# Performance work log

Hardware: AMD Instinct MI355X
Metric: run time of the kernel (lower is better)

## Reference

```python
import jax, jax.numpy as jnp
import numpy as np

N_LAYERS = 12
N_HEADS = 12
D_MODEL = 768
VOCAB = 50257
T_WIN = 1024
B, T = 4, 1024
STD = 0.02


def setup_inputs() -> dict:
    key = jax.random.key(0)
    ks = jax.random.split(key, 8)
    inp = jax.random.randint(ks[0], (B, T), 0, VOCAB)
    target = jax.random.randint(ks[1], (B, T), 0, VOCAB)
    wte = jax.random.normal(ks[2], (VOCAB, D_MODEL), jnp.float32) * STD
    wpe = jax.random.normal(ks[3], (T_WIN, D_MODEL), jnp.float32) * STD
    attn_w = jax.random.normal(ks[4], (N_LAYERS, D_MODEL, 3 * D_MODEL), jnp.float32) * STD
    proj_w = jax.random.normal(ks[5], (N_LAYERS, D_MODEL, D_MODEL), jnp.float32) * STD
    fc_w = jax.random.normal(ks[6], (N_LAYERS, D_MODEL, 4 * D_MODEL), jnp.float32) * STD
    fc2_w = jax.random.normal(ks[7], (N_LAYERS, 4 * D_MODEL, D_MODEL), jnp.float32) * STD
    return {
        'inp': inp, 'target': target, 'wte': wte, 'wpe': wpe,
        'ln1_w': jnp.ones((N_LAYERS, D_MODEL), jnp.float32),
        'ln1_b': jnp.zeros((N_LAYERS, D_MODEL), jnp.float32),
        'attn_w': attn_w,
        'attn_b': jnp.zeros((N_LAYERS, 3 * D_MODEL), jnp.float32),
        'proj_w': proj_w,
        'proj_b': jnp.zeros((N_LAYERS, D_MODEL), jnp.float32),
        'ln2_w': jnp.ones((N_LAYERS, D_MODEL), jnp.float32),
        'ln2_b': jnp.zeros((N_LAYERS, D_MODEL), jnp.float32),
        'fc_w': fc_w,
        'fc_b': jnp.zeros((N_LAYERS, 4 * D_MODEL), jnp.float32),
        'fc2_w': fc2_w,
        'fc2_b': jnp.zeros((N_LAYERS, D_MODEL), jnp.float32),
        'lnf_w': jnp.ones((D_MODEL,), jnp.float32),
        'lnf_b': jnp.zeros((D_MODEL,), jnp.float32),
    }


def _layernorm(x, w, b, eps=1e-5):
    mu = jnp.mean(x, axis=-1, keepdims=True)
    var = jnp.var(x, axis=-1, keepdims=True)
    return (x - mu) * jax.lax.rsqrt(var + eps) * w + b


def _attention(x, w_qkv, b_qkv, w_proj, b_proj):
    b, t, c = x.shape
    hd = c // N_HEADS
    qkv = x @ w_qkv + b_qkv                      # [B,T,3C]
    q, k, v = jnp.split(qkv, 3, axis=-1)
    # [B,H,T,hd]
    q = q.reshape(b, t, N_HEADS, hd).transpose(0, 2, 1, 3)
    k = k.reshape(b, t, N_HEADS, hd).transpose(0, 2, 1, 3)
    v = v.reshape(b, t, N_HEADS, hd).transpose(0, 2, 1, 3)
    scores = jnp.einsum('bhqd,bhkd->bhqk', q, k) / jnp.sqrt(jnp.float32(hd))
    causal = jnp.tril(jnp.ones((t, t), bool))
    scores = jnp.where(causal[None, None], scores, -jnp.inf)
    w = jax.nn.softmax(scores, axis=-1)          # dropout p=0 (eval)
    ctx = jnp.einsum('bhqk,bhkd->bhqd', w, v)
    ctx = ctx.transpose(0, 2, 1, 3).reshape(b, t, c)
    return ctx @ w_proj + b_proj


def reference(inp, target, wte, wpe, ln1_w, ln1_b, attn_w, attn_b, proj_w, proj_b,
              ln2_w, ln2_b, fc_w, fc_b, fc2_w, fc2_b, lnf_w, lnf_b):
    b, t = inp.shape
    x = wte[inp] + wpe[:t][None]                 # [B,T,C]
    for i in range(N_LAYERS):
        x = x + _attention(_layernorm(x, ln1_w[i], ln1_b[i]),
                           attn_w[i], attn_b[i], proj_w[i], proj_b[i])
        h = _layernorm(x, ln2_w[i], ln2_b[i])
        h = jax.nn.gelu(h @ fc_w[i] + fc_b[i], approximate=True)
        x = x + (h @ fc2_w[i] + fc2_b[i])
    x = _layernorm(x, lnf_w, lnf_b)
    logits = x @ wte.T                            # tied lm_head, no bias
    logp = jax.nn.log_softmax(logits, axis=-1)
    nll = -jnp.take_along_axis(logp, target[..., None], axis=-1)[..., 0]
    loss = jnp.mean(nll)
    return logits, loss
```

## Files before the change

kernel.cpp:

```cpp
#include <hip/hip_runtime.h>
#include <hip/hip_bf16.h>
#include <cmath>

#define NLAYERS 12
#define NHEADS  12
#define DM      768
#define VOCAB   50257
#define TSEQ    1024
#define BT      4096
#define NCHUNK  786

typedef __attribute__((ext_vector_type(4))) float f32x4;
typedef __attribute__((ext_vector_type(8))) short bf16x8;
typedef __attribute__((ext_vector_type(4))) short s16x4;

typedef __hip_bfloat16 bf16;

#define MFMA16(a, b, c) __builtin_amdgcn_mfma_f32_16x16x32_bf16(a, b, c, 0, 0, 0)

__device__ __forceinline__ void gload16(const void* g, void* l) {
    __builtin_amdgcn_global_load_lds(
        (const __attribute__((address_space(1))) void*)g,
        (__attribute__((address_space(3))) void*)l, 16, 0, 0);
}

__device__ __forceinline__ void wg_barrier() {
    asm volatile("" ::: "memory");
    __builtin_amdgcn_s_barrier();
    asm volatile("" ::: "memory");
}

__device__ __forceinline__ float gelu_tanh(float v) {
    float u = 0.7978845608028654f * (v + 0.044715f * v * v * v);
    return 0.5f * v * (1.0f + tanhf(u));
}

__device__ __forceinline__ short f2bf(float f) {
    bf16 h = (bf16)f;
    return *reinterpret_cast<short*>(&h);
}

struct ushort4s { short a, b, c, d; };

__global__ void transpose_bf16_kernel(const float* __restrict__ in, bf16* __restrict__ out,
                                      int K, int N) {
    __shared__ float tile[32][33];
    size_t lofs = (size_t)blockIdx.z * K * N;
    int k0 = blockIdx.y * 32, n0 = blockIdx.x * 32;
    int tx = threadIdx.x, ty = threadIdx.y;
#pragma unroll
    for (int i = 0; i < 32; i += 8)
        tile[ty + i][tx] = in[lofs + (size_t)(k0 + ty + i) * N + n0 + tx];
    __syncthreads();
#pragma unroll
    for (int i = 0; i < 32; i += 8)
        out[lofs + (size_t)(n0 + ty + i) * K + k0 + tx] = (bf16)tile[tx][ty + i];
}

__global__ void tobf16_kernel(const float* __restrict__ in, bf16* __restrict__ out, size_t n) {
    size_t i = (size_t)blockIdx.x * 256 + threadIdx.x;
    if (i < n) out[i] = (bf16)in[i];
}

__global__ void embed_kernel(const int* __restrict__ inp, const float* __restrict__ wte,
                             const float* __restrict__ wpe, float* __restrict__ x) {
    int idx = blockIdx.x * 256 + threadIdx.x;
    int m = idx / (DM / 4), c4 = idx % (DM / 4);
    int tok = inp[m];
    int t = m & (TSEQ - 1);
    float4 a = reinterpret_cast<const float4*>(wte)[(size_t)tok * (DM / 4) + c4];
    float4 b = reinterpret_cast<const float4*>(wpe)[(size_t)t * (DM / 4) + c4];
    float4 o = {a.x + b.x, a.y + b.y, a.z + b.z, a.w + b.w};
    reinterpret_cast<float4*>(x)[idx] = o;
}

__global__ __launch_bounds__(256) void ln_kernel(const float* __restrict__ x,
                                                 const float* __restrict__ w,
                                                 const float* __restrict__ b,
                                                 bf16* __restrict__ y) {
    int tid = threadIdx.x, wv = tid >> 6, lane = tid & 63;
    int row = blockIdx.x * 4 + wv;
    const float4* xr = reinterpret_cast<const float4*>(x + (size_t)row * DM);
    float4 v[3];
    float s = 0.f, q = 0.f;
#pragma unroll
    for (int j = 0; j < 3; ++j) {
        v[j] = xr[lane + 64 * j];
        s += v[j].x + v[j].y + v[j].z + v[j].w;
        q += v[j].x * v[j].x + v[j].y * v[j].y + v[j].z * v[j].z + v[j].w * v[j].w;
    }
#pragma unroll
    for (int o = 1; o < 64; o <<= 1) { s += __shfl_xor(s, o); q += __shfl_xor(q, o); }
    float mu  = s * (1.0f / DM);
    float var = q * (1.0f / DM) - mu * mu;
    float inv = rsqrtf(var + 1e-5f);
#pragma unroll
    for (int j = 0; j < 3; ++j) {
        int c4 = lane + 64 * j;
        float4 wv4 = reinterpret_cast<const float4*>(w)[c4];
        float4 bv4 = reinterpret_cast<const float4*>(b)[c4];
        ushort4s o;
        o.a = f2bf((v[j].x - mu) * inv * wv4.x + bv4.x);
        o.b = f2bf((v[j].y - mu) * inv * wv4.y + bv4.y);
        o.c = f2bf((v[j].z - mu) * inv * wv4.z + bv4.z);
        o.d = f2bf((v[j].w - mu) * inv * wv4.w + bv4.w);
        *reinterpret_cast<ushort4s*>(y + (size_t)row * DM + c4 * 4) = o;
    }
}

#define GF_GELU    1
#define GF_OBF16   2
#define GF_CLAMP   4
#define GF_PARTIAL 8

template<int FLAGS, int TAG>
__global__ __launch_bounds__(256) void gemm_k(
    const bf16* __restrict__ A, const bf16* __restrict__ Bt,
    const float* __restrict__ bias, const float* __restrict__ resid,
    void* __restrict__ C, float2* __restrict__ partials,
    int M, int N, int K) {
    __shared__ short ldsA[2][128 * 32];
    __shared__ short ldsB[2][128 * 32];
    int tid = threadIdx.x;
    int lane = tid & 63, w = tid >> 6;
    int wm = w >> 1, wn = w & 1;
    int r = lane & 15, kq = lane >> 4;
    int bm = blockIdx.x * 128, bn = blockIdx.y * 128;

    f32x4 acc[4][4] = {};

    auto stage = [&](int buf, int k0) {
#pragma unroll
        for (int i = 0; i < 2; ++i) {
            int chunk = i * 256 + tid;
            int row = chunk >> 2;
            int gs = (chunk & 3) ^ ((row >> 1) & 3);
            const bf16* ga = A + (size_t)(bm + row) * K + k0 + gs * 8;
            gload16(ga, &ldsA[buf][(i * 256 + w * 64) * 8]);
            int brow = bn + row;
            if (FLAGS & GF_CLAMP) brow = min(brow, N - 1);
            const bf16* gb = Bt + (size_t)brow * K + k0 + gs * 8;
            gload16(gb, &ldsB[buf][(i * 256 + w * 64) * 8]);
        }
    };
    auto compute = [&](int buf) {
        bf16x8 af[4], bfr[4];
#pragma unroll
        for (int m = 0; m < 4; ++m) {
            int row = wm * 64 + m * 16 + r;
            af[m] = *reinterpret_cast<bf16x8*>(&ldsA[buf][row * 32 + (kq ^ ((row >> 1) & 3)) * 8]);
        }
#pragma unroll
        for (int n = 0; n < 4; ++n) {
            int row = wn * 64 + n * 16 + r;
            bfr[n] = *reinterpret_cast<bf16x8*>(&ldsB[buf][row * 32 + (kq ^ ((row >> 1) & 3)) * 8]);
        }
#pragma unroll
        for (int m = 0; m < 4; ++m)
#pragma unroll
            for (int n = 0; n < 4; ++n)
                acc[m][n] = MFMA16(af[m], bfr[n], acc[m][n]);
    };

    stage(0, 0);
    __syncthreads();
    int buf = 0;
    for (int k0 = 32; k0 < K; k0 += 32) {
        stage(buf ^ 1, k0);
        compute(buf);
        __syncthreads();
        buf ^= 1;
    }
    compute(buf);

    int row0 = bm + wm * 64, col0 = bn + wn * 64;
#pragma unroll
    for (int m = 0; m < 4; ++m) {
#pragma unroll
        for (int n = 0; n < 4; ++n) {
            int col = col0 + n * 16 + r;
            if (col < N) {
#pragma unroll
                for (int rr = 0; rr < 4; ++rr) {
                    int row = row0 + m * 16 + kq * 4 + rr;
                    float v = acc[m][n][rr];
                    if (bias) v += bias[col];
                    if (FLAGS & GF_GELU) v = gelu_tanh(v);
                    if (resid) v += resid[(size_t)row * N + col];
                    if (FLAGS & GF_OBF16) ((bf16*)C)[(size_t)row * N + col] = (bf16)v;
                    else                  ((float*)C)[(size_t)row * N + col] = v;
                }
            }
        }
    }
}

template<int FLAGS, int TAG>
__global__ __launch_bounds__(512, 1) void gemm256_8p(
    const bf16* __restrict__ A, const bf16* __restrict__ Bt,
    const float* __restrict__ bias, const float* __restrict__ resid,
    void* __restrict__ C, float2* __restrict__ partials,
    int M, int N, int K) {
    __shared__ short lds[2][2][256 * 64];
    int tid = threadIdx.x;
    int lane = tid & 63, w = tid >> 6;
    int wm = w >> 2, wn = w & 3;
    int r = lane & 15, kq = lane >> 4;
    int bm = blockIdx.x * 256, bn = blockIdx.y * 256;

    f32x4 acc[8][4] = {};

    auto stage_half = [&](int buf, int kt, int half) {
        int mat = half >> 1;
        int hrow = (half & 1) * 128;
        const bf16* src = mat ? Bt : A;
        int base = mat ? bn : bm;
#pragma unroll
        for (int i = 0; i < 2; ++i) {
            int chunk = i * 512 + tid;
            int lrow = hrow + (chunk >> 3);
            int gsrc = (chunk & 7) ^ (lrow & 7);
            int grow = base + lrow;
            if (mat && (FLAGS & GF_CLAMP)) grow = min(grow, N - 1);
            gload16(src + (size_t)grow * K + kt * 64 + gsrc * 8,
                    &lds[buf][mat][hrow * 64 + chunk * 8]);
        }
    };

    auto do_phase = [&](int buf, int p) {
        int mh = p >> 1, nh = p & 1;
        bf16x8 bfr[2][2], af[4][2];
#pragma unroll
        for (int n2 = 0; n2 < 2; ++n2) {
            int row = wn * 64 + (nh * 2 + n2) * 16 + r;
#pragma unroll
            for (int kk = 0; kk < 2; ++kk)
                bfr[n2][kk] = *reinterpret_cast<bf16x8*>(
                    &lds[buf][1][row * 64 + ((kk * 4 + kq) ^ (row & 7)) * 8]);
        }
#pragma unroll
        for (int m2 = 0; m2 < 4; ++m2) {
            int row = wm * 128 + (mh * 4 + m2) * 16 + r;
#pragma unroll
            for (int kk = 0; kk < 2; ++kk)
                af[m2][kk] = *reinterpret_cast<bf16x8*>(
                    &lds[buf][0][row * 64 + ((kk * 4 + kq) ^ (row & 7)) * 8]);
        }
        __builtin_amdgcn_s_setprio(1);
#pragma unroll
        for (int m2 = 0; m2 < 4; ++m2)
#pragma unroll
            for (int n2 = 0; n2 < 2; ++n2)
#pragma unroll
                for (int kk = 0; kk < 2; ++kk)
                    acc[mh * 4 + m2][nh * 2 + n2] =
                        MFMA16(af[m2][kk], bfr[n2][kk], acc[mh * 4 + m2][nh * 2 + n2]);
        __builtin_amdgcn_s_setprio(0);
    };

    const int NT = K / 64;
    stage_half(0, 0, 0); stage_half(0, 0, 1); stage_half(0, 0, 2); stage_half(0, 0, 3);
    for (int t = 0; t < NT; ++t) {
        int buf = t & 1;
        bool more = (t + 1 < NT);
        if (more) { stage_half(buf ^ 1, t + 1, 0); stage_half(buf ^ 1, t + 1, 1); }
        if (more) asm volatile("s_waitcnt vmcnt(4)" ::: "memory");
        else      asm volatile("s_waitcnt vmcnt(0)" ::: "memory");
        wg_barrier();
        do_phase(buf, 0);
        wg_barrier();
        if (more) { stage_half(buf ^ 1, t + 1, 2); stage_half(buf ^ 1, t + 1, 3); }
        do_phase(buf, 1);
        wg_barrier();
        do_phase(buf, 2);
        wg_barrier();
        do_phase(buf, 3);
        wg_barrier();
    }

    int row0 = bm + wm * 128, col0 = bn + wn * 64;
#pragma unroll
    for (int m = 0; m < 8; ++m) {
#pragma unroll
        for (int n = 0; n < 4; ++n) {
            int col = col0 + n * 16 + r;
            if (col < N) {
#pragma unroll
                for (int rr = 0; rr < 4; ++rr) {
                    int row = row0 + m * 16 + kq * 4 + rr;
                    float v = acc[m][n][rr];
                    if (bias) v += bias[col];
                    if (FLAGS & GF_GELU) v = gelu_tanh(v);
                    if (resid) v += resid[(size_t)row * N + col];
                    if (FLAGS & GF_OBF16) ((bf16*)C)[(size_t)row * N + col] = (bf16)v;
                    else                  ((float*)C)[(size_t)row * N + col] = v;
                }
            }
        }
    }

    if (FLAGS & GF_PARTIAL) {
        int chunk = (bn >> 6) + wn;
        if (chunk < NCHUNK) {
#pragma unroll
            for (int m = 0; m < 8; ++m) {
#pragma unroll
                for (int rr = 0; rr < 4; ++rr) {
                    float vals[4], mx = -INFINITY;
#pragma unroll
                    for (int n = 0; n < 4; ++n) {
                        int col = col0 + n * 16 + r;
                        float v = (col < N) ? acc[m][n][rr] : -INFINITY;
                        vals[n] = v;
                        mx = fmaxf(mx, v);
                    }
#pragma unroll
                    for (int o = 1; o < 16; o <<= 1) mx = fmaxf(mx, __shfl_xor(mx, o));
                    float sum = 0.f;
#pragma unroll
                    for (int n = 0; n < 4; ++n)
                        if (vals[n] > -INFINITY) sum += __expf(vals[n] - mx);
#pragma unroll
                    for (int o = 1; o < 16; o <<= 1) sum += __shfl_xor(sum, o);
                    if (r == 0) {
                        int row = row0 + m * 16 + kq * 4 + rr;
                        partials[(size_t)row * NCHUNK + chunk] = make_float2(mx, sum);
                    }
                }
            }
        }
    }
}

__global__ __launch_bounds__(256) void flash_attn_kernel(const bf16* __restrict__ qkv,
                                                         bf16* __restrict__ ctx) {
    __shared__ short Ks[128 * 64];
    __shared__ short Vt[64 * 128];
    __shared__ short Ps[4][16][132];

    int tid = threadIdx.x, lane = tid & 63, w = tid >> 6;
    int r = lane & 15, kq = lane >> 4;
    int q0 = blockIdx.x * 64;
    int bh = blockIdx.y;
    int b = bh / NHEADS, h = bh % NHEADS;
    const int RS = 3 * DM;

    const bf16* qbase = qkv + (size_t)(b * TSEQ + q0 + w * 16 + r) * RS + h * 64;
    bf16x8 qf[2];
    qf[0] = *reinterpret_cast<const bf16x8*>(qbase + kq * 8);
    qf[1] = *reinterpret_cast<const bf16x8*>(qbase + 32 + kq * 8);

    f32x4 of[4] = {};
    float mrow[4] = {-INFINITY, -INFINITY, -INFINITY, -INFINITY};
    float lrow[4] = {};

    int kvq = tid >> 3;
    int d0 = (tid & 7) * 8;
    const bf16* kbase0 = qkv + (size_t)(b * TSEQ) * RS + DM + h * 64;
    const bf16* vbase0 = qkv + (size_t)(b * TSEQ) * RS + 2 * DM + h * 64;
    bf16x8 kr0, kr1, kr2, kr3, vr0, vr1, vr2, vr3;

    auto loadKV = [&](int t) {
        const bf16* kb = kbase0 + (size_t)(t * 128 + kvq * 4) * RS + d0;
        const bf16* vb = vbase0 + (size_t)(t * 128 + kvq * 4) * RS + d0;
        kr0 = *reinterpret_cast<const bf16x8*>(kb);
        kr1 = *reinterpret_cast<const bf16x8*>(kb + RS);
        kr2 = *reinterpret_cast<const bf16x8*>(kb + 2 * RS);
        kr3 = *reinterpret_cast<const bf16x8*>(kb + 3 * RS);
        vr0 = *reinterpret_cast<const bf16x8*>(vb);
        vr1 = *reinterpret_cast<const bf16x8*>(vb + RS);
        vr2 = *reinterpret_cast<const bf16x8*>(vb + 2 * RS);
        vr3 = *reinterpret_cast<const bf16x8*>(vb + 3 * RS);
    };
    auto writeKV = [&]() {
        bf16x8 krs[4] = {kr0, kr1, kr2, kr3};
#pragma unroll
        for (int j = 0; j < 4; ++j) {
            int kv = kvq * 4 + j;
            int pg = (tid & 7) ^ (kv & 7);
            *reinterpret_cast<bf16x8*>(&Ks[kv * 64 + pg * 8]) = krs[j];
        }
        int lg = kvq >> 1, half = kvq & 1;
#pragma unroll
        for (int jj = 0; jj < 8; ++jj) {
            int d = d0 + jj;
            int phys = lg ^ (d & 7);
            s16x4 pk = {vr0[jj], vr1[jj], vr2[jj], vr3[jj]};
            *reinterpret_cast<s16x4*>(&Vt[d * 128 + phys * 8 + half * 4]) = pk;
        }
    };

    int ntiles = (blockIdx.x >> 1) + 1;
    loadKV(0);
    for (int t = 0; t < ntiles; ++t) {
        __syncthreads();
        writeKV();
        __syncthreads();
        if (t + 1 < ntiles) loadKV(t + 1);

        int kv0 = t * 128;
        f32x4 sf[8];
#pragma unroll
        for (int n = 0; n < 8; ++n) sf[n] = (f32x4){0.f, 0.f, 0.f, 0.f};
        __builtin_amdgcn_s_setprio(1);
#pragma unroll
        for (int n = 0; n < 8; ++n) {
            int row = n * 16 + r;
#pragma unroll
            for (int kt = 0; kt < 2; ++kt) {
                int gran = (kt * 4 + kq) ^ (row & 7);
                bf16x8 kf = *reinterpret_cast<bf16x8*>(&Ks[row * 64 + gran * 8]);
                sf[n] = MFMA16(qf[kt], kf, sf[n]);
            }
        }
        __builtin_amdgcn_s_setprio(0);

        bool diag = (kv0 + 128 > q0);
        float alpha[4];
#pragma unroll
        for (int rr = 0; rr < 4; ++rr) {
            int qrow = q0 + w * 16 + kq * 4 + rr;
            float vals[8];
            float mx = mrow[rr];
#pragma unroll
            for (int n = 0; n < 8; ++n) {
                float v = sf[n][rr] * 0.125f;
                if (diag && (kv0 + n * 16 + r) > qrow) v = -INFINITY;
                vals[n] = v;
                mx = fmaxf(mx, v);
            }
#pragma unroll
            for (int o = 1; o < 16; o <<= 1) mx = fmaxf(mx, __shfl_xor(mx, o));
            float al = __expf(mrow[rr] - mx);
            float sum = 0.f;
#pragma unroll
            for (int n = 0; n < 8; ++n) {
                float p = __expf(vals[n] - mx);
                vals[n] = p;
                sum += p;
            }
#pragma unroll
            for (int o = 1; o < 16; o <<= 1) sum += __shfl_xor(sum, o);
            mrow[rr] = mx;
            lrow[rr] = lrow[rr] * al + sum;
            alpha[rr] = al;
#pragma unroll
            for (int n = 0; n < 8; ++n) Ps[w][kq * 4 + rr][n * 16 + r] = f2bf(vals[n]);
        }
#pragma unroll
        for (int n = 0; n < 4; ++n)
#pragma unroll
            for (int rr = 0; rr < 4; ++rr) of[n][rr] *= alpha[rr];

        __builtin_amdgcn_s_setprio(1);
#pragma unroll
        for (int kt = 0; kt < 4; ++kt) {
            bf16x8 pa = *reinterpret_cast<bf16x8*>(&Ps[w][r][kt * 32 + kq * 8]);
#pragma unroll
            for (int n = 0; n < 4; ++n) {
                int row = n * 16 + r;
                int gran = (kt * 4 + kq) ^ (row & 7);
                bf16x8 vf = *reinterpret_cast<bf16x8*>(&Vt[row * 128 + gran * 8]);
                of[n] = MFMA16(pa, vf, of[n]);
            }
        }
        __builtin_amdgcn_s_setprio(0);
    }

#pragma unroll
    for (int rr = 0; rr < 4; ++rr) {
        float inv = 1.0f / lrow[rr];
        int qrow = q0 + w * 16 + kq * 4 + rr;
        bf16* cb = ctx + (size_t)(b * TSEQ + qrow) * DM + h * 64;
#pragma unroll
        for (int n = 0; n < 4; ++n) cb[n * 16 + r] = (bf16)(of[n][rr] * inv);
    }
}

__global__ __launch_bounds__(256) void loss_reduce_kernel(const float2* __restrict__ partials,
                                                          const float* __restrict__ logits,
                                                          const int* __restrict__ target,
                                                          float* __restrict__ nll) {
    int row = blockIdx.x, tid = threadIdx.x;
    const float2* pr = partials + (size_t)row * NCHUNK;
    float m = -INFINITY, s = 0.f;
    for (int c = tid; c < NCHUNK; c += 256) {
        float2 p = pr[c];
        if (p.x > m) { s = s * __expf(m - p.x) + p.y; m = p.x; }
        else         { s += p.y * __expf(p.x - m); }
    }
    __shared__ float sm[256], ssum[256];
    sm[tid] = m; ssum[tid] = s; __syncthreads();
    for (int o = 128; o; o >>= 1) {
        if (tid < o) {
            float m2 = sm[tid + o], s2 = ssum[tid + o];
            float mm = fmaxf(sm[tid], m2);
            ssum[tid] = ssum[tid] * __expf(sm[tid] - mm) + s2 * __expf(m2 - mm);
            sm[tid] = mm;
        }
        __syncthreads();
    }
    if (tid == 0) {
        float lse = sm[0] + logf(ssum[0]);
        nll[row] = lse - logits[(size_t)row * VOCAB + target[row]];
    }
}

__global__ void loss2_kernel(const float* __restrict__ nll, float* __restrict__ loss) {
    int tid = threadIdx.x;
    float s = 0.f;
    for (int i = tid; i < BT; i += 1024) s += nll[i];
    __shared__ float r[1024];
    r[tid] = s; __syncthreads();
    for (int o = 512; o; o >>= 1) { if (tid < o) r[tid] += r[tid + o]; __syncthreads(); }
    if (tid == 0) *loss = r[0] * (1.0f / BT);
}

extern "C" void kernel_launch(void* const* d_in, const int* in_sizes, int n_in,
                              void* d_out, int out_size, void* d_ws, size_t ws_size,
                              hipStream_t stream) {
    const int*   inp    = (const int*)  d_in[0];
    const int*   target = (const int*)  d_in[1];
    const float* wte    = (const float*)d_in[2];
    const float* wpe    = (const float*)d_in[3];
    const float* ln1_w  = (const float*)d_in[4];
    const float* ln1_b  = (const float*)d_in[5];
    const float* attn_w = (const float*)d_in[6];
    const float* attn_b = (const float*)d_in[7];
    const float* proj_w = (const float*)d_in[8];
    const float* proj_b = (const float*)d_in[9];
    const float* ln2_w  = (const float*)d_in[10];
    const float* ln2_b  = (const float*)d_in[11];
    const float* fc_w   = (const float*)d_in[12];
    const float* fc_b   = (const float*)d_in[13];
    const float* fc2_w  = (const float*)d_in[14];
    const float* fc2_b  = (const float*)d_in[15];
    const float* lnf_w  = (const float*)d_in[16];
    const float* lnf_b  = (const float*)d_in[17];
    float* out = (float*)d_out;

    char* p = (char*)d_ws;
    auto alloc = [&](size_t bytes) { char* q = p; p += (bytes + 255) & ~(size_t)255; return q; };
    float* x     = (float*)alloc((size_t)BT * DM * 4);
    float* nll   = (float*)alloc((size_t)BT * 4);
    bf16*  qkvb  = (bf16*) alloc((size_t)BT * 3 * DM * 2);
    bf16*  tmpb  = (bf16*) alloc((size_t)BT * DM * 2);
    bf16*  ctxb  = (bf16*) alloc((size_t)BT * DM * 2);
    bf16*  hb    = (bf16*) alloc((size_t)BT * 4 * DM * 2);
    bf16*  wteb  = (bf16*) alloc((size_t)VOCAB * DM * 2);
    bf16*  wqkvT = (bf16*) alloc((size_t)NLAYERS * 3 * DM * DM * 2);
    bf16*  wprojT= (bf16*) alloc((size_t)NLAYERS * DM * DM * 2);
    bf16*  wfcT  = (bf16*) alloc((size_t)NLAYERS * 4 * DM * DM * 2);
    bf16*  wfc2T = (bf16*) alloc((size_t)NLAYERS * 4 * DM * DM * 2);
    float2* partials = (float2*)ctxb;

    dim3 tb(32, 8);
    transpose_bf16_kernel<<<dim3(3 * DM / 32, DM / 32, NLAYERS), tb, 0, stream>>>(attn_w, wqkvT, DM, 3 * DM);
    transpose_bf16_kernel<<<dim3(DM / 32, DM / 32, NLAYERS), tb, 0, stream>>>(proj_w, wprojT, DM, DM);
    transpose_bf16_kernel<<<dim3(4 * DM / 32, DM / 32, NLAYERS), tb, 0, stream>>>(fc_w, wfcT, DM, 4 * DM);
    transpose_bf16_kernel<<<dim3(DM / 32, 4 * DM / 32, NLAYERS), tb, 0, stream>>>(fc2_w, wfc2T, 4 * DM, DM);
    {
        size_t n = (size_t)VOCAB * DM;
        tobf16_kernel<<<(unsigned)((n + 255) / 256), 256, 0, stream>>>(wte, wteb, n);
    }

    embed_kernel<<<BT * DM / 4 / 256, 256, 0, stream>>>(inp, wte, wpe, x);

    for (int i = 0; i < NLAYERS; ++i) {
        ln_kernel<<<BT / 4, 256, 0, stream>>>(x, ln1_w + i * DM, ln1_b + i * DM, tmpb);
        gemm_k<GF_OBF16, 0><<<dim3(BT / 128, 3 * DM / 128), 256, 0, stream>>>(
            tmpb, wqkvT + (size_t)i * 3 * DM * DM, attn_b + i * 3 * DM, nullptr,
            qkvb, nullptr, BT, 3 * DM, DM);
        flash_attn_kernel<<<dim3(TSEQ / 64, 4 * NHEADS), 256, 0, stream>>>(qkvb, ctxb);
        gemm_k<0, 1><<<dim3(BT / 128, DM / 128), 256, 0, stream>>>(
            ctxb, wprojT + (size_t)i * DM * DM, proj_b + i * DM, x,
            x, nullptr, BT, DM, DM);
        ln_kernel<<<BT / 4, 256, 0, stream>>>(x, ln2_w + i * DM, ln2_b + i * DM, tmpb);
        gemm_k<GF_GELU | GF_OBF16, 2><<<dim3(BT / 128, 4 * DM / 128), 256, 0, stream>>>(
            tmpb, wfcT + (size_t)i * 4 * DM * DM, fc_b + i * 4 * DM, nullptr,
            hb, nullptr, BT, 4 * DM, DM);
        gemm_k<0, 3><<<dim3(BT / 128, DM / 128), 256, 0, stream>>>(
            hb, wfc2T + (size_t)i * 4 * DM * DM, fc2_b + i * DM, x,
            x, nullptr, BT, DM, 4 * DM);
    }

    ln_kernel<<<BT / 4, 256, 0, stream>>>(x, lnf_w, lnf_b, tmpb);
    gemm256_8p<GF_CLAMP | GF_PARTIAL, 4><<<dim3(BT / 256, (VOCAB + 255) / 256), 512, 0, stream>>>(
        tmpb, wteb, nullptr, nullptr, out, partials, BT, VOCAB, DM);
    loss_reduce_kernel<<<BT, 256, 0, stream>>>(partials, out, target, nll);
    loss2_kernel<<<1, 1024, 0, stream>>>(nll, out + (size_t)out_size - 1);
}
```

Measured before the change: 4.262 ms.

## Replace LM-head GEMM with 128x256 tile kernel and widen flash attention blocks

The 256x256 eight-phase LM-head GEMM is replaced by a 128x256 tile kernel with K-step 32, which runs several blocks per CU and uses a simpler double-buffered pipeline. Flash attention now uses 512 threads over 128-query tiles, splits K and V staging between the two halves of the block, and launches the longest causal tiles first to balance load. gemm_k's epilogue drops its column bounds check and clamp, which is only safe because its shapes divide evenly. The changes trade the large LM-head tile's reuse for occupancy, and the attention rework may raise register and LDS pressure.

```diff
diff --git a/kernel.cpp b/kernel.cpp
--- a/kernel.cpp
+++ b/kernel.cpp
@@ -138,7 +138,6 @@
             const bf16* ga = A + (size_t)(bm + row) * K + k0 + gs * 8;
             gload16(ga, &ldsA[buf][(i * 256 + w * 64) * 8]);
             int brow = bn + row;
-            if (FLAGS & GF_CLAMP) brow = min(brow, N - 1);
             const bf16* gb = Bt + (size_t)brow * K + k0 + gs * 8;
             gload16(gb, &ldsB[buf][(i * 256 + w * 64) * 8]);
         }
@@ -172,6 +171,98 @@
         buf ^= 1;
     }
     compute(buf);
+
+    int row0 = bm + wm * 64, col0 = bn + wn * 64;
+#pragma unroll
+    for (int m = 0; m < 4; ++m) {
+#pragma unroll
+        for (int n = 0; n < 4; ++n) {
+            int col = col0 + n * 16 + r;
+#pragma unroll
+            for (int rr = 0; rr < 4; ++rr) {
+                int row = row0 + m * 16 + kq * 4 + rr;
+                float v = acc[m][n][rr];
+                if (bias) v += bias[col];
+                if (FLAGS & GF_GELU) v = gelu_tanh(v);
+                if (resid) v += resid[(size_t)row * N + col];
+                if (FLAGS & GF_OBF16) ((bf16*)C)[(size_t)row * N + col] = (bf16)v;
+                else                  ((float*)C)[(size_t)row * N + col] = v;
+            }
+        }
+    }
+}
+
+template<int FLAGS, int TAG>
+__global__ __launch_bounds__(512, 4) void gemm_wide(
+    const bf16* __restrict__ A, const bf16* __restrict__ Bt,
+    const float* __restrict__ bias, const float* __restrict__ resid,
+    void* __restrict__ C, float2* __restrict__ partials,
+    int M, int N, int K) {
+    __shared__ short ldsA[2][128 * 32];
+    __shared__ short ldsB[2][256 * 32];
+    int tid = threadIdx.x;
+    int lane = tid & 63, w = tid >> 6;
+    int wm = w >> 2, wn = w & 3;
+    int r = lane & 15, kq = lane >> 4;
+    int bm = blockIdx.x * 128, bn = blockIdx.y * 256;
+
+    f32x4 acc[4][4] = {};
+
+    auto stage = [&](int buf, int kt) {
+        int k0 = kt * 32;
+        {
+            int row = tid >> 2;
+            int gs = (tid & 3) ^ ((row >> 1) & 3);
+            gload16(A + (size_t)(bm + row) * K + k0 + gs * 8, &ldsA[buf][tid * 8]);
+        }
+#pragma unroll
+        for (int i = 0; i < 2; ++i) {
+            int chunk = i * 512 + tid;
+            int row = chunk >> 2;
+            int gs = (chunk & 3) ^ ((row >> 1) & 3);
+            int grow = bn + row;
+            if (FLAGS & GF_CLAMP) grow = min(grow, N - 1);
+            gload16(Bt + (size_t)grow * K + k0 + gs * 8, &ldsB[buf][chunk * 8]);
+        }
+    };
+    auto compute = [&](int buf) {
+        bf16x8 af[4], bfr[4];
+#pragma unroll
+        for (int m = 0; m < 4; ++m) {
+            int row = wm * 64 + m * 16 + r;
+            af[m] = *reinterpret_cast<bf16x8*>(&ldsA[buf][row * 32 + (kq ^ ((row >> 1) & 3)) * 8]);
+        }
+#pragma unroll
+        for (int n = 0; n < 4; ++n) {
+            int row = wn * 64 + n * 16 + r;
+            bfr[n] = *reinterpret_cast<bf16x8*>(&ldsB[buf][row * 32 + (kq ^ ((row >> 1) & 3)) * 8]);
+        }
+        __builtin_amdgcn_s_setprio(1);
+#pragma unroll
+        for (int m = 0; m < 4; ++m)
+#pragma unroll
+            for (int n = 0; n < 4; ++n)
+                acc[m][n] = MFMA16(af[m], bfr[n], acc[m][n]);
+        __builtin_amdgcn_s_setprio(0);
+    };
+
+    const int NT = K / 32;
+    stage(0, 0);
+    asm volatile("s_waitcnt vmcnt(0)" ::: "memory");
+    wg_barrier();
+    for (int t = 0; t < NT; ++t) {
+        int buf = t & 1;
+        bool more = (t + 1 < NT);
+        if (more) {
+            stage(buf ^ 1, t + 1);
+            asm volatile("s_waitcnt vmcnt(3)" ::: "memory");
+        } else {
+            asm volatile("s_waitcnt vmcnt(0)" ::: "memory");
+        }
+        wg_barrier();
+        compute(buf);
+        wg_barrier();
+    }
 
     int row0 = bm + wm * 64, col0 = bn + wn * 64;
 #pragma unroll
@@ -193,117 +284,12 @@
             }
         }
     }
-}
-
-template<int FLAGS, int TAG>
-__global__ __launch_bounds__(512, 1) void gemm256_8p(
-    const bf16* __restrict__ A, const bf16* __restrict__ Bt,
-    const float* __restrict__ bias, const float* __restrict__ resid,
-    void* __restrict__ C, float2* __restrict__ partials,
-    int M, int N, int K) {
-    __shared__ short lds[2][2][256 * 64];
-    int tid = threadIdx.x;
-    int lane = tid & 63, w = tid >> 6;
-    int wm = w >> 2, wn = w & 3;
-    int r = lane & 15, kq = lane >> 4;
-    int bm = blockIdx.x * 256, bn = blockIdx.y * 256;
-
-    f32x4 acc[8][4] = {};
-
-    auto stage_half = [&](int buf, int kt, int half) {
-        int mat = half >> 1;
-        int hrow = (half & 1) * 128;
-        const bf16* src = mat ? Bt : A;
-        int base = mat ? bn : bm;
-#pragma unroll
-        for (int i = 0; i < 2; ++i) {
-            int chunk = i * 512 + tid;
-            int lrow = hrow + (chunk >> 3);
-            int gsrc = (chunk & 7) ^ (lrow & 7);
-            int grow = base + lrow;
-            if (mat && (FLAGS & GF_CLAMP)) grow = min(grow, N - 1);
-            gload16(src + (size_t)grow * K + kt * 64 + gsrc * 8,
-                    &lds[buf][mat][hrow * 64 + chunk * 8]);
-        }
-    };
-
-    auto do_phase = [&](int buf, int p) {
-        int mh = p >> 1, nh = p & 1;
-        bf16x8 bfr[2][2], af[4][2];
-#pragma unroll
-        for (int n2 = 0; n2 < 2; ++n2) {
-            int row = wn * 64 + (nh * 2 + n2) * 16 + r;
-#pragma unroll
-            for (int kk = 0; kk < 2; ++kk)
-                bfr[n2][kk] = *reinterpret_cast<bf16x8*>(
-                    &lds[buf][1][row * 64 + ((kk * 4 + kq) ^ (row & 7)) * 8]);
-        }
-#pragma unroll
-        for (int m2 = 0; m2 < 4; ++m2) {
-            int row = wm * 128 + (mh * 4 + m2) * 16 + r;
-#pragma unroll
-            for (int kk = 0; kk < 2; ++kk)
-                af[m2][kk] = *reinterpret_cast<bf16x8*>(
-                    &lds[buf][0][row * 64 + ((kk * 4 + kq) ^ (row & 7)) * 8]);
-        }
-        __builtin_amdgcn_s_setprio(1);
-#pragma unroll
-        for (int m2 = 0; m2 < 4; ++m2)
-#pragma unroll
-            for (int n2 = 0; n2 < 2; ++n2)
-#pragma unroll
-                for (int kk = 0; kk < 2; ++kk)
-                    acc[mh * 4 + m2][nh * 2 + n2] =
-                        MFMA16(af[m2][kk], bfr[n2][kk], acc[mh * 4 + m2][nh * 2 + n2]);
-        __builtin_amdgcn_s_setprio(0);
-    };
-
-    const int NT = K / 64;
-    stage_half(0, 0, 0); stage_half(0, 0, 1); stage_half(0, 0, 2); stage_half(0, 0, 3);
-    for (int t = 0; t < NT; ++t) {
-        int buf = t & 1;
-        bool more = (t + 1 < NT);
-        if (more) { stage_half(buf ^ 1, t + 1, 0); stage_half(buf ^ 1, t + 1, 1); }
-        if (more) asm volatile("s_waitcnt vmcnt(4)" ::: "memory");
-        else      asm volatile("s_waitcnt vmcnt(0)" ::: "memory");
-        wg_barrier();
-        do_phase(buf, 0);
-        wg_barrier();
-        if (more) { stage_half(buf ^ 1, t + 1, 2); stage_half(buf ^ 1, t + 1, 3); }
-        do_phase(buf, 1);
-        wg_barrier();
-        do_phase(buf, 2);
-        wg_barrier();
-        do_phase(buf, 3);
-        wg_barrier();
-    }
-
-    int row0 = bm + wm * 128, col0 = bn + wn * 64;
-#pragma unroll
-    for (int m = 0; m < 8; ++m) {
-#pragma unroll
-        for (int n = 0; n < 4; ++n) {
-            int col = col0 + n * 16 + r;
-            if (col < N) {
-#pragma unroll
-                for (int rr = 0; rr < 4; ++rr) {
-                    int row = row0 + m * 16 + kq * 4 + rr;
-                    float v = acc[m][n][rr];
-                    if (bias) v += bias[col];
-                    if (FLAGS & GF_GELU) v = gelu_tanh(v);
-                    if (resid) v += resid[(size_t)row * N + col];
-                    if (FLAGS & GF_OBF16) ((bf16*)C)[(size_t)row * N + col] = (bf16)v;
-                    else                  ((float*)C)[(size_t)row * N + col] = v;
-                }
-            }
-        }
-    }
 
     if (FLAGS & GF_PARTIAL) {
         int chunk = (bn >> 6) + wn;
         if (chunk < NCHUNK) {
 #pragma unroll
-            for (int m = 0; m < 8; ++m) {
+            for (int m = 0; m < 4; ++m) {
 #pragma unroll
                 for (int rr = 0; rr < 4; ++rr) {
                     float vals[4], mx = -INFINITY;
@@ -332,15 +318,16 @@
     }
 }
 
-__global__ __launch_bounds__(256) void flash_attn_kernel(const bf16* __restrict__ qkv,
-                                                         bf16* __restrict__ ctx) {
+__global__ __launch_bounds__(512, 4) void flash_attn_kernel(const bf16* __restrict__ qkv,
+                                                            bf16* __restrict__ ctx) {
     __shared__ short Ks[128 * 64];
     __shared__ short Vt[64 * 128];
-    __shared__ short Ps[4][16][132];
+    __shared__ short Ps[8][16][132];
 
     int tid = threadIdx.x, lane = tid & 63, w = tid >> 6;
     int r = lane & 15, kq = lane >> 4;
-    int q0 = blockIdx.x * 64;
+    int qt = (int)gridDim.x - 1 - (int)blockIdx.x;
+    int q0 = qt * 128;
     int bh = blockIdx.y;
     int b = bh / NHEADS, h = bh % NHEADS;
     const int RS = 3 * DM;
@@ -354,43 +341,42 @@
     float mrow[4] = {-INFINITY, -INFINITY, -INFINITY, -INFINITY};
     float lrow[4] = {};
 
-    int kvq = tid >> 3;
-    int d0 = (tid & 7) * 8;
-    const bf16* kbase0 = qkv + (size_t)(b * TSEQ) * RS + DM + h * 64;
-    const bf16* vbase0 = qkv + (size_t)(b * TSEQ) * RS + 2 * DM + h * 64;
-    bf16x8 kr0, kr1, kr2, kr3, vr0, vr1, vr2, vr3;
+    int stid = tid & 255;
+    int kvq = stid >> 3;
+    int d0 = (stid & 7) * 8;
+    bool isK = tid < 256;
+    const bf16* sb0 = qkv + (size_t)(b * TSEQ) * RS + (isK ? DM : 2 * DM) + h * 64;
+    bf16x8 r0, r1, r2, r3;
 
     auto loadKV = [&](int t) {
-        const bf16* kb = kbase0 + (size_t)(t * 128 + kvq * 4) * RS + d0;
-        const bf16* vb = vbase0 + (size_t)(t * 128 + kvq * 4) * RS + d0;
-        kr0 = *reinterpret_cast<const bf16x8*>(kb);
-        kr1 = *reinterpret_cast<const bf16x8*>(kb + RS);
-        kr2 = *reinterpret_cast<const bf16x8*>(kb + 2 * RS);
-        kr3 = *reinterpret_cast<const bf16x8*>(kb + 3 * RS);
-        vr0 = *reinterpret_cast<const bf16x8*>(vb);
-        vr1 = *reinterpret_cast<const bf16x8*>(vb + RS);
-        vr2 = *reinterpret_cast<const bf16x8*>(vb + 2 * RS);
-        vr3 = *reinterpret_cast<const bf16x8*>(vb + 3 * RS);
+        const bf16* p = sb0 + (size_t)(t * 128 + kvq * 4) * RS + d0;
+        r0 = *reinterpret_cast<const bf16x8*>(p);
+        r1 = *reinterpret_cast<const bf16x8*>(p + RS);
+        r2 = *reinterpret_cast<const bf16x8*>(p + 2 * RS);
+        r3 = *reinterpret_cast<const bf16x8*>(p + 3 * RS);
     };
     auto writeKV = [&]() {
-        bf16x8 krs[4] = {kr0, kr1, kr2, kr3};
-#pragma unroll
-        for (int j = 0; j < 4; ++j) {
-            int kv = kvq * 4 + j;
-            int pg = (tid & 7) ^ (kv & 7);
-            *reinterpret_cast<bf16x8*>(&Ks[kv * 64 + pg * 8]) = krs[j];
-        }
-        int lg = kvq >> 1, half = kvq & 1;
-#pragma unroll
-        for (int jj = 0; jj < 8; ++jj) {
-            int d = d0 + jj;
-            int phys = lg ^ (d & 7);
-            s16x4 pk = {vr0[jj], vr1[jj], vr2[jj], vr3[jj]};
-            *reinterpret_cast<s16x4*>(&Vt[d * 128 + phys * 8 + half * 4]) = pk;
+        if (isK) {
+            bf16x8 rs[4] = {r0, r1, r2, r3};
+#pragma unroll
+            for (int j = 0; j < 4; ++j) {
+                int kv = kvq * 4 + j;
+                int pg = (stid & 7) ^ (kv & 7);
+                *reinterpret_cast<bf16x8*>(&Ks[kv * 64 + pg * 8]) = rs[j];
+            }
+        } else {
+            int lg = kvq >> 1, half = kvq & 1;
+#pragma unroll
+            for (int jj = 0; jj < 8; ++jj) {
+                int d = d0 + jj;
+                int phys = lg ^ (d & 7);
+                s16x4 pk = {r0[jj], r1[jj], r2[jj], r3[jj]};
+                *reinterpret_cast<s16x4*>(&Vt[d * 128 + phys * 8 + half * 4]) = pk;
+            }
         }
     };
 
-    int ntiles = (blockIdx.x >> 1) + 1;
+    int ntiles = qt + 1;
     loadKV(0);
     for (int t = 0; t < ntiles; ++t) {
         __syncthreads();
@@ -571,7 +557,7 @@
         gemm_k<GF_OBF16, 0><<<dim3(BT / 128, 3 * DM / 128), 256, 0, stream>>>(
             tmpb, wqkvT + (size_t)i * 3 * DM * DM, attn_b + i * 3 * DM, nullptr,
             qkvb, nullptr, BT, 3 * DM, DM);
-        flash_attn_kernel<<<dim3(TSEQ / 64, 4 * NHEADS), 256, 0, stream>>>(qkvb, ctxb);
+        flash_attn_kernel<<<dim3(TSEQ / 128, 4 * NHEADS), 512, 0, stream>>>(qkvb, ctxb);
         gemm_k<0, 1><<<dim3(BT / 128, DM / 128), 256, 0, stream>>>(
             ctxb, wprojT + (size_t)i * DM * DM, proj_b + i * DM, x,
             x, nullptr, BT, DM, DM);
@@ -585,7 +571,7 @@
     }
 
     ln_kernel<<<BT / 4, 256, 0, stream>>>(x, lnf_w, lnf_b, tmpb);
-    gemm256_8p<GF_CLAMP | GF_PARTIAL, 4><<<dim3(BT / 256, (VOCAB + 255) / 256), 512, 0, stream>>>(
+    gemm_wide<GF_CLAMP | GF_PARTIAL, 4><<<dim3(BT / 128, (VOCAB + 255) / 256), 512, 0, stream>>>(
         tmpb, wteb, nullptr, nullptr, out, partials, BT, VOCAB, DM);
     loss_reduce_kernel<<<BT, 256, 0, stream>>>(partials, out, target, nll);
     loss2_kernel<<<1, 1024, 0, stream>>>(nll, out + (size_t)out_size - 1);
```

Result: no change. 4.242 ms (-0.5%).
